# Optimization experiments

Hardware: AMD Instinct MI355X
Metric: run time of the kernel (lower is better)

Reference implementation:

```python
import jax, jax.numpy as jnp
import numpy as np

EPS = 1e-7  # keras.backend.epsilon()
B, U, F = 1024, 256, 31
D = 1 + U + F  # features dim after concat


def setup_inputs() -> dict:
    key = jax.random.key(0)
    ks = jax.random.split(key, 9)
    s = 1.0 / np.sqrt(D)
    return {
        "last_cell": jax.random.uniform(ks[0], (B, U), dtype=jnp.float32),
        "input_precipitation": jax.random.uniform(ks[1], (B,), dtype=jnp.float32),
        "input_other_features": jax.random.normal(ks[2], (B, F), dtype=jnp.float32),
        "W_i": jax.random.normal(ks[3], (D, U), dtype=jnp.float32) * s,
        "b_i": jnp.zeros((U,), dtype=jnp.float32),
        "W_r": jax.random.normal(ks[4], (D, U * U), dtype=jnp.float32) * s,
        "b_r": jnp.zeros((U * U,), dtype=jnp.float32),
        "W_o": jax.random.normal(ks[5], (D, U), dtype=jnp.float32) * s,
        "b_o": jnp.zeros((U,), dtype=jnp.float32),
    }


def reference(last_cell, input_precipitation, input_other_features,
              W_i, b_i, W_r, b_r, W_o, b_o):
    # L1-normalize last cell state (mass fractions)
    l1 = jnp.sum(jnp.abs(last_cell), axis=-1, keepdims=True) + EPS
    last_cell_hat = last_cell / l1
    p = input_precipitation[:, None]  # [B,1]
    features = jnp.concatenate([p, last_cell_hat, input_other_features], axis=-1)  # [B,D]

    # input gate: sigmoid then L1-normalized across units (mass-conserving split)
    ig = jax.nn.sigmoid(features @ W_i + b_i)
    ig = ig / jnp.sum(jnp.abs(ig), axis=-1, keepdims=True)

    # redistribution matrix: relu, reshape [B,U,U], L1-normalize each row
    R = jax.nn.relu(features @ W_r + b_r).reshape(-1, U, U)
    R = R / jnp.sum(jnp.abs(R), axis=-1, keepdims=True)

    # output gate: sigmoid
    og = jax.nn.sigmoid(features @ W_o + b_o)

    cell_in = ig * p                                   # [B,U]
    cell_sys = jnp.einsum('bu,buv->bv', last_cell, R)  # batched (1xU)@(UxU)
    candidate = cell_in + cell_sys
    output = og * candidate
    cell = (1.0 - og) * candidate
    return (cell, output)
```

## Files before the change

kernel.cpp:

```cpp
#include <hip/hip_runtime.h>


#define EPS_L1 1e-7f

constexpr int BB  = 1024;
constexpr int U   = 256;
constexpr int F   = 31;
constexpr int D   = 1 + U + F;
constexpr int NBV = BB * U;
constexpr int NCH = D / 32;
constexpr int UIMGB = NCH * 16384;
constexpr size_t WTB_BYTES  = (size_t)258 * UIMGB;
constexpr size_t FEAT_BYTES = (size_t)BB * D * 2;
constexpr size_t PART_BYTES = (size_t)32 * BB * U * 4;
constexpr size_t NEED_PRIV  = WTB_BYTES + FEAT_BYTES + PART_BYTES;
constexpr int PITCH = 260;

typedef float f32x4 __attribute__((ext_vector_type(4)));
typedef short bf16x8 __attribute__((ext_vector_type(8)));

__device__ __forceinline__ unsigned f2bf(float x) {
  union { float f; unsigned u; } v; v.f = x;
  unsigned r = v.u + 0x7FFFu + ((v.u >> 16) & 1u);
  return r >> 16;
}

#define GLDS16(gp, lp)                                                        \
  __builtin_amdgcn_global_load_lds(                                          \
      (const __attribute__((address_space(1))) void*)(gp),                   \
      (__attribute__((address_space(3))) void*)(lp), 16, 0, 0)

#define MFMA16(a, b, c) __builtin_amdgcn_mfma_f32_16x16x32_bf16((a), (b), (c), 0, 0, 0)

__global__ __launch_bounds__(256) void k_prep(
    const float* __restrict__ lc, const float* __restrict__ p,
    const float* __restrict__ other,
    const float* __restrict__ Wi, const float* __restrict__ Wr,
    const float* __restrict__ Wo,
    short* __restrict__ WtB, short* __restrict__ featImg,
    float* __restrict__ partial) {
  __shared__ short lds[2][32 * PITCH];
  __shared__ float inv_s[64];
  const int bid = blockIdx.x, t = threadIdx.x;

  if (bid < 774) {
    const int u = bid / 3, part = bid % 3;
    const float* src; long ld;
    if (u < 256)       { src = Wr + (size_t)u * 256; ld = 65536; }
    else if (u == 256) { src = Wi; ld = 256; }
    else               { src = Wo; ld = 256; }
    short* dst = WtB + (size_t)u * 73728;
    const int lane = t & 63, wave = t >> 6;
    const int g = lane >> 4, l15 = lane & 15;

#pragma unroll
    for (int cc = 0; cc < 3; ++cc) {
      const int c = part * 3 + cc;
      short* buf = lds[cc & 1];
#pragma unroll
      for (int i = 0; i < 8; ++i) {
        const int f = i * 256 + t;
        const int row = f >> 6, col4 = f & 63;
        const float4 v = *(const float4*)(src + (size_t)(c * 32 + row) * ld + col4 * 4);
        const unsigned lo = f2bf(v.x) | (f2bf(v.y) << 16);
        const unsigned hi = f2bf(v.z) | (f2bf(v.w) << 16);
        unsigned* wp = (unsigned*)&buf[row * PITCH + col4 * 4];
        wp[0] = lo; wp[1] = hi;
      }
      __syncthreads();
#pragma unroll
      for (int i = 0; i < 4; ++i) {
        const int n0 = wave * 4 + i;
        bf16x8 h;
#pragma unroll
        for (int j = 0; j < 8; ++j)
          h[j] = buf[(g * 8 + j) * PITCH + n0 * 16 + l15];
        *(bf16x8*)(dst + (size_t)(c * 16 + n0) * 512 + lane * 8) = h;
      }
      __syncthreads();
    }
  } else if (bid < 790) {
    const int mb = bid - 774;
    const int b0 = mb * 64;
    const int row = t >> 2, q = t & 3;
    const float4* lp = (const float4*)(lc + (size_t)(b0 + row) * 256 + q * 64);
    float s = 0.f;
#pragma unroll
    for (int j = 0; j < 16; ++j) {
      const float4 v = lp[j];
      s += fabsf(v.x) + fabsf(v.y) + fabsf(v.z) + fabsf(v.w);
    }
    s += __shfl_xor(s, 1, 64);
    s += __shfl_xor(s, 2, 64);
    if (q == 0) inv_s[row] = 1.f / (s + EPS_L1);
    __syncthreads();
#pragma unroll
    for (int i = 0; i < 9; ++i) {
      const int idx = i * 256 + t;
      const int reg = idx >> 6, l = idx & 63;
      const int c = reg >> 2, mt = reg & 3;
      const int lrow = mt * 16 + (l & 15);
      const int grow = b0 + lrow;
      const int k0 = c * 32 + (l >> 4) * 8;
      bf16x8 h;
#pragma unroll
      for (int j = 0; j < 8; ++j) {
        const int k = k0 + j;
        float v;
        if (k == 0) v = p[grow];
        else if (k <= 256) v = lc[(size_t)grow * 256 + (k - 1)] * inv_s[lrow];
        else v = other[(size_t)grow * 31 + (k - 257)];
        h[j] = (short)f2bf(v);
      }
      *(bf16x8*)(featImg + (size_t)mb * 18432 + (size_t)reg * 512 + l * 8) = h;
    }
  } else {
    float4* cs4 = (float4*)partial;
    const int base = (bid - 790) * 8192 + t;
    const float4 z = {0.f, 0.f, 0.f, 0.f};
#pragma unroll
    for (int k2 = 0; k2 < 32; ++k2) cs4[base + k2 * 256] = z;
  }
}

template <bool PRIV>
__global__ __launch_bounds__(1024, 4) void k_heavyR7(
    const short* __restrict__ featImg, const short* __restrict__ WtB,
    const float* __restrict__ lc, const float* __restrict__ br,
    float* __restrict__ partial) {
  __shared__ short aT[36864];
  __shared__ float rsum[2][128][12];
  __shared__ float lcs[2][128];

  const int t = threadIdx.x, lane = t & 63, wave = t >> 6;
  const int cq = wave & 7, rh = wave >> 3;
  const int quad = lane >> 4, l15 = lane & 15;
  const int bid = blockIdx.x;
  const int Mb = bid >> 5, ug = bid & 31;
  const int b0 = Mb * 128, u0 = ug * 8;

  {
    const char* gA = (const char*)featImg + (size_t)Mb * 73728;
    char* lA = (char*)aT;
#pragma unroll
    for (int i = 0; i < 5; ++i) {
      const int off = i * 16384 + t * 16;
      if (off < 73728) GLDS16(gA + off, lA + off);
    }
  }

  const char* aB = (const char*)aT + rh * 36864 + lane * 16;
  const char* bB = (const char*)WtB + (size_t)u0 * UIMGB + cq * 2048 + lane * 16;

  f32x4 acc[4][2], outa[4][2];
#pragma unroll
  for (int m = 0; m < 4; ++m)
#pragma unroll
    for (int n = 0; n < 2; ++n)
#pragma unroll
      for (int r = 0; r < 4; ++r) { acc[m][n][r] = 0.f; outa[m][n][r] = 0.f; }

  bf16x8 afr[2][4], bfr[2][2];

#pragma unroll
  for (int n = 0; n < 2; ++n) bfr[0][n] = *(const bf16x8*)(bB + n * 1024);

  __syncthreads();

#pragma unroll
  for (int m = 0; m < 4; ++m) afr[0][m] = *(const bf16x8*)(aB + m * 1024);

  for (int uu = 0; uu < 8; ++uu) {
    const int u = u0 + uu;
    float bv[2];

#pragma unroll
    for (int c = 0; c < 9; ++c) {
      if (c == 0) {
#pragma unroll
        for (int n = 0; n < 2; ++n)
          bv[n] = br[(size_t)u * 256 + cq * 32 + n * 16 + l15];
        if (t < 128) lcs[uu & 1][t] = lc[(size_t)(b0 + t) * 256 + u];
      }
      if (c < 8) {
#pragma unroll
        for (int n = 0; n < 2; ++n)
          bfr[(c + 1) & 1][n] = *(const bf16x8*)(bB + (c + 1) * 16384 + n * 1024);
#pragma unroll
        for (int m = 0; m < 4; ++m)
          afr[(c + 1) & 1][m] = *(const bf16x8*)(aB + (c + 1) * 4096 + m * 1024);
      }
#pragma unroll
      for (int m = 0; m < 4; ++m)
#pragma unroll
        for (int n = 0; n < 2; ++n)
          acc[m][n] = MFMA16(afr[c & 1][m], bfr[c & 1][n], acc[m][n]);
    }
    bB += UIMGB;

#pragma unroll
    for (int n = 0; n < 2; ++n) bfr[0][n] = *(const bf16x8*)(bB + n * 1024);
#pragma unroll
    for (int m = 0; m < 4; ++m) afr[0][m] = *(const bf16x8*)(aB + m * 1024);

    const int ub = uu & 1;
    float sm[4][4];
#pragma unroll
    for (int m = 0; m < 4; ++m)
#pragma unroll
      for (int r = 0; r < 4; ++r) {
        float sv = 0.f;
#pragma unroll
        for (int n = 0; n < 2; ++n) {
          const float rv = fmaxf(acc[m][n][r] + bv[n], 0.f);
          acc[m][n][r] = rv;
          sv += rv;
        }
        sm[m][r] = sv;
      }
#pragma unroll
    for (int msk = 1; msk < 16; msk <<= 1)
#pragma unroll
      for (int m = 0; m < 4; ++m)
#pragma unroll
        for (int r = 0; r < 4; ++r)
          sm[m][r] += __shfl_xor(sm[m][r], msk, 64);
    if (l15 == 0) {
#pragma unroll
      for (int m = 0; m < 4; ++m)
#pragma unroll
        for (int r = 0; r < 4; ++r)
          rsum[ub][rh * 64 + m * 16 + quad * 4 + r][cq] = sm[m][r];
    }
    __syncthreads();
#pragma unroll
    for (int m = 0; m < 4; ++m)
#pragma unroll
      for (int r = 0; r < 4; ++r) {
        const int row = rh * 64 + m * 16 + quad * 4 + r;
        const float4 ra = *(const float4*)&rsum[ub][row][0];
        const float4 rb = *(const float4*)&rsum[ub][row][4];
        const float tot = ((ra.x + ra.y) + (ra.z + ra.w)) +
                          ((rb.x + rb.y) + (rb.z + rb.w));
        const float alpha = lcs[ub][row] * __builtin_amdgcn_rcpf(tot);
#pragma unroll
        for (int n = 0; n < 2; ++n) {
          outa[m][n][r] = fmaf(alpha, acc[m][n][r], outa[m][n][r]);
          acc[m][n][r] = 0.f;
        }
      }
  }

  const size_t pb = PRIV ? ((size_t)ug << 18) : 0;
#pragma unroll
  for (int m = 0; m < 4; ++m)
#pragma unroll
    for (int r = 0; r < 4; ++r) {
      const int grow = b0 + rh * 64 + m * 16 + quad * 4 + r;
      const size_t rb = pb + (size_t)grow * 256 + cq * 32 + l15;
      if (PRIV) {
        partial[rb]      = outa[m][0][r];
        partial[rb + 16] = outa[m][1][r];
      } else {
        atomicAdd(&partial[rb],      outa[m][0][r]);
        atomicAdd(&partial[rb + 16], outa[m][1][r]);
      }
    }
}

__global__ __launch_bounds__(512, 2) void k_postR7(
    const short* __restrict__ featImg, const short* __restrict__ WtB,
    const float* __restrict__ bi, const float* __restrict__ bo,
    const float* __restrict__ p, const float* __restrict__ partial, int npart,
    float* __restrict__ dout) {
  __shared__ short aT9[9 * 512];
  __shared__ float cs[16 * 256];
  __shared__ float rsum[16][12];
  __shared__ float ps[16];

  const int t = threadIdx.x, lane = t & 63, cg = t >> 6;
  const int quad = lane >> 4, l15 = lane & 15;
  const int mb16 = blockIdx.x, b0 = mb16 * 16;
  const int mb = mb16 >> 2, mt = mb16 & 3;

  {
    const char* gsrc = (const char*)featImg + (size_t)mb * 36864 + mt * 1024;
    char* ldst = (char*)aT9;
    GLDS16(gsrc + (size_t)(t >> 6) * 4096 + (t & 63) * 16, ldst + t * 16);
    if (t < 64)
      GLDS16(gsrc + (size_t)8 * 4096 + t * 16, ldst + 8192 + t * 16);
  }
  if (t < 16) ps[t] = p[b0 + t];

  {
    const float* pbase = partial + (size_t)b0 * 256;
    f32x4 s0 = {0.f, 0.f, 0.f, 0.f}, s1 = {0.f, 0.f, 0.f, 0.f};
#pragma unroll 4
    for (int ug = 0; ug < npart; ++ug) {
      const f32x4* pp = (const f32x4*)(pbase + (size_t)ug * 262144);
      s0 += pp[t];
      s1 += pp[512 + t];
    }
    ((f32x4*)cs)[t] = s0;
    ((f32x4*)cs)[512 + t] = s1;
  }

  f32x4 acc[2];
#pragma unroll
  for (int n = 0; n < 2; ++n)
#pragma unroll
    for (int r = 0; r < 4; ++r) acc[n][r] = 0.f;

  const char* bptr = (const char*)WtB + (size_t)256 * UIMGB + cg * 2048 + lane * 16;
  bf16x8 cb0 = *(const bf16x8*)(bptr);
  bf16x8 cb1 = *(const bf16x8*)(bptr + 1024);
  bf16x8 nb0 = *(const bf16x8*)(bptr + 16384);
  bf16x8 nb1 = *(const bf16x8*)(bptr + 16384 + 1024);
  bptr += 32768;

  __syncthreads();

  float ig0[4], ig1[4], og0[4], og1[4];

#pragma unroll
  for (int g = 0; g < 2; ++g) {
    const float* bias = (g == 0) ? bi : bo;
    const float bv0 = bias[cg * 32 + l15];
    const float bv1 = bias[cg * 32 + 16 + l15];
#pragma unroll
    for (int c = 0; c < 9; ++c) {
      const bf16x8 pb0 = *(const bf16x8*)(bptr);
      const bf16x8 pb1 = *(const bf16x8*)(bptr + 1024);
      bptr += 16384;
      const bf16x8 a0 = *(const bf16x8*)((const char*)aT9 + c * 1024 + lane * 16);
      acc[0] = MFMA16(a0, cb0, acc[0]);
      acc[1] = MFMA16(a0, cb1, acc[1]);
      cb0 = nb0; cb1 = nb1; nb0 = pb0; nb1 = pb1;
    }

#pragma unroll
    for (int r = 0; r < 4; ++r) {
      const float v0 = 1.f / (1.f + __expf(-(acc[0][r] + bv0)));
      const float v1 = 1.f / (1.f + __expf(-(acc[1][r] + bv1)));
      if (g == 0) { ig0[r] = v0; ig1[r] = v1; }
      else        { og0[r] = v0; og1[r] = v1; }
      acc[0][r] = 0.f;
      acc[1][r] = 0.f;
    }

    if (g == 0) {
      float sm[4];
#pragma unroll
      for (int r = 0; r < 4; ++r) sm[r] = ig0[r] + ig1[r];
#pragma unroll
      for (int msk = 1; msk < 16; msk <<= 1)
#pragma unroll
        for (int r = 0; r < 4; ++r)
          sm[r] += __shfl_xor(sm[r], msk, 64);
      if (l15 == 0) {
#pragma unroll
        for (int r = 0; r < 4; ++r)
          rsum[quad * 4 + r][cg] = sm[r];
      }
      __syncthreads();
#pragma unroll
      for (int r = 0; r < 4; ++r) {
        const int row = quad * 4 + r;
        const float4 ra = *(const float4*)&rsum[row][0];
        const float4 rb = *(const float4*)&rsum[row][4];
        const float inv = 1.f / (((ra.x + ra.y) + (ra.z + ra.w)) +
                                 ((rb.x + rb.y) + (rb.z + rb.w)));
        ig0[r] *= inv;
        ig1[r] *= inv;
      }
    }
  }

#pragma unroll
  for (int r = 0; r < 4; ++r) {
    const int row = quad * 4 + r;
    const float pr = ps[row];
    const int ci = row * 256 + cg * 32 + l15;
    const size_t base = (size_t)(b0 + row) * 256 + cg * 32 + l15;
    {
      const float cand = fmaf(ig0[r], pr, cs[ci]);
      dout[base] = (1.f - og0[r]) * cand;
      dout[NBV + base] = og0[r] * cand;
    }
    {
      const float cand = fmaf(ig1[r], pr, cs[ci + 16]);
      dout[base + 16] = (1.f - og1[r]) * cand;
      dout[NBV + base + 16] = og1[r] * cand;
    }
  }
}

extern "C" void kernel_launch(void* const* d_in, const int* in_sizes, int n_in,
                              void* d_out, int out_size, void* d_ws, size_t ws_size,
                              hipStream_t stream) {
  const float* lc    = (const float*)d_in[0];
  const float* p     = (const float*)d_in[1];
  const float* other = (const float*)d_in[2];
  const float* Wi    = (const float*)d_in[3];
  const float* bi    = (const float*)d_in[4];
  const float* Wr    = (const float*)d_in[5];
  const float* br    = (const float*)d_in[6];
  const float* Wo    = (const float*)d_in[7];
  const float* bo    = (const float*)d_in[8];
  float* out = (float*)d_out;

  char* wsb = (char*)d_ws;
  short* WtB      = (short*)wsb;
  short* featImg  = (short*)(wsb + WTB_BYTES);
  float* partial  = (float*)(wsb + WTB_BYTES + FEAT_BYTES);
  const bool priv = (ws_size >= NEED_PRIV);

  k_prep<<<798, 256, 0, stream>>>(lc, p, other, Wi, Wr, Wo, WtB, featImg, partial);
  if (priv)
    k_heavyR7<true><<<256, 1024, 0, stream>>>(featImg, WtB, lc, br, partial);
  else
    k_heavyR7<false><<<256, 1024, 0, stream>>>(featImg, WtB, lc, br, partial);
  k_postR7<<<64, 512, 0, stream>>>(featImg, WtB, bi, bo, p, partial,
                                   priv ? 32 : 1, out);
}
```

Before: 249.0 us.

## Restructure weight prep, widen heavy kernel tiles, drop private partials for atomics

The weight-transpose prep now uses one block per (unit, chunk) with a bf16-pair packed LDS transpose, giving about three times as many blocks. The heavy kernel moves from 1024 to 512 threads, so each wave covers 64 output columns (4 N fragments), with triple-buffered B fragments and last_cell values preloaded once. The 32-way private partial buffer is removed. All blocks now atomically add into a single zeroed cell_sys array, which the post kernel reads directly instead of summing 32 partials. This trades a large partial-buffer write and read for more atomics and higher register pressure per wave.

Result: faster. 216.8 us (-12.9%).

```diff
diff --git a/kernel.cpp b/kernel.cpp
--- a/kernel.cpp
+++ b/kernel.cpp
@@ -12,9 +12,6 @@
 constexpr int UIMGB = NCH * 16384;
 constexpr size_t WTB_BYTES  = (size_t)258 * UIMGB;
 constexpr size_t FEAT_BYTES = (size_t)BB * D * 2;
-constexpr size_t PART_BYTES = (size_t)32 * BB * U * 4;
-constexpr size_t NEED_PRIV  = WTB_BYTES + FEAT_BYTES + PART_BYTES;
-constexpr int PITCH = 260;
 
 typedef float f32x4 __attribute__((ext_vector_type(4)));
 typedef short bf16x8 __attribute__((ext_vector_type(8)));
@@ -38,49 +35,47 @@
     const float* __restrict__ Wi, const float* __restrict__ Wr,
     const float* __restrict__ Wo,
     short* __restrict__ WtB, short* __restrict__ featImg,
-    float* __restrict__ partial) {
-  __shared__ short lds[2][32 * PITCH];
+    float* __restrict__ cell_sys) {
+  __shared__ unsigned tw[256][17];
   __shared__ float inv_s[64];
   const int bid = blockIdx.x, t = threadIdx.x;
 
-  if (bid < 774) {
-    const int u = bid / 3, part = bid % 3;
+  if (bid < 2322) {
+    const int u = bid / 9, c = bid % 9;
     const float* src; long ld;
     if (u < 256)       { src = Wr + (size_t)u * 256; ld = 65536; }
     else if (u == 256) { src = Wi; ld = 256; }
     else               { src = Wo; ld = 256; }
-    short* dst = WtB + (size_t)u * 73728;
+
+    const int kp = t >> 4, f = t & 15;
+    const float* r0 = src + (size_t)(c * 32 + 2 * kp) * ld;
+    const float* r1 = r0 + ld;
+#pragma unroll
+    for (int i = 0; i < 4; ++i) {
+      const int v0 = f * 4 + i * 64;
+      const float4 a = *(const float4*)(r0 + v0);
+      const float4 b = *(const float4*)(r1 + v0);
+      tw[v0 + 0][kp] = f2bf(a.x) | (f2bf(b.x) << 16);
+      tw[v0 + 1][kp] = f2bf(a.y) | (f2bf(b.y) << 16);
+      tw[v0 + 2][kp] = f2bf(a.z) | (f2bf(b.z) << 16);
+      tw[v0 + 3][kp] = f2bf(a.w) | (f2bf(b.w) << 16);
+    }
+    __syncthreads();
+
     const int lane = t & 63, wave = t >> 6;
     const int g = lane >> 4, l15 = lane & 15;
-
-#pragma unroll
-    for (int cc = 0; cc < 3; ++cc) {
-      const int c = part * 3 + cc;
-      short* buf = lds[cc & 1];
-#pragma unroll
-      for (int i = 0; i < 8; ++i) {
-        const int f = i * 256 + t;
-        const int row = f >> 6, col4 = f & 63;
-        const float4 v = *(const float4*)(src + (size_t)(c * 32 + row) * ld + col4 * 4);
-        const unsigned lo = f2bf(v.x) | (f2bf(v.y) << 16);
-        const unsigned hi = f2bf(v.z) | (f2bf(v.w) << 16);
-        unsigned* wp = (unsigned*)&buf[row * PITCH + col4 * 4];
-        wp[0] = lo; wp[1] = hi;
-      }
-      __syncthreads();
-#pragma unroll
-      for (int i = 0; i < 4; ++i) {
-        const int n0 = wave * 4 + i;
-        bf16x8 h;
-#pragma unroll
-        for (int j = 0; j < 8; ++j)
-          h[j] = buf[(g * 8 + j) * PITCH + n0 * 16 + l15];
-        *(bf16x8*)(dst + (size_t)(c * 16 + n0) * 512 + lane * 8) = h;
-      }
-      __syncthreads();
-    }
-  } else if (bid < 790) {
-    const int mb = bid - 774;
+    short* dst = WtB + (size_t)u * 73728 + (size_t)c * 16 * 512;
+#pragma unroll
+    for (int ii = 0; ii < 4; ++ii) {
+      const int n0 = wave * 4 + ii;
+      const int row = n0 * 16 + l15;
+      union { unsigned u4[4]; bf16x8 h; } cv;
+#pragma unroll
+      for (int j = 0; j < 4; ++j) cv.u4[j] = tw[row][g * 4 + j];
+      *(bf16x8*)(dst + (size_t)n0 * 512 + lane * 8) = cv.h;
+    }
+  } else if (bid < 2338) {
+    const int mb = bid - 2322;
     const int b0 = mb * 64;
     const int row = t >> 2, q = t & 3;
     const float4* lp = (const float4*)(lc + (size_t)(b0 + row) * 256 + q * 64);
@@ -115,25 +110,24 @@
       *(bf16x8*)(featImg + (size_t)mb * 18432 + (size_t)reg * 512 + l * 8) = h;
     }
   } else {
-    float4* cs4 = (float4*)partial;
-    const int base = (bid - 790) * 8192 + t;
+    float4* cs4 = (float4*)cell_sys;
+    const int base = (bid - 2338) * 8192 + t;
     const float4 z = {0.f, 0.f, 0.f, 0.f};
 #pragma unroll
     for (int k2 = 0; k2 < 32; ++k2) cs4[base + k2 * 256] = z;
   }
 }
 
-template <bool PRIV>
-__global__ __launch_bounds__(1024, 4) void k_heavyR7(
+__global__ __launch_bounds__(512, 2) void k_heavyR8(
     const short* __restrict__ featImg, const short* __restrict__ WtB,
     const float* __restrict__ lc, const float* __restrict__ br,
-    float* __restrict__ partial) {
+    float* __restrict__ cell_sys) {
   __shared__ short aT[36864];
-  __shared__ float rsum[2][128][12];
-  __shared__ float lcs[2][128];
+  __shared__ float rsum[2][128][4];
+  __shared__ float lcs[8][128];
 
   const int t = threadIdx.x, lane = t & 63, wave = t >> 6;
-  const int cq = wave & 7, rh = wave >> 3;
+  const int cq = wave & 3, rh = wave >> 2;
   const int quad = lane >> 4, l15 = lane & 15;
   const int bid = blockIdx.x;
   const int Mb = bid >> 5, ug = bid & 31;
@@ -143,49 +137,56 @@
     const char* gA = (const char*)featImg + (size_t)Mb * 73728;
     char* lA = (char*)aT;
 #pragma unroll
-    for (int i = 0; i < 5; ++i) {
-      const int off = i * 16384 + t * 16;
-      if (off < 73728) GLDS16(gA + off, lA + off);
-    }
+    for (int i = 0; i < 9; ++i)
+      GLDS16(gA + i * 8192 + t * 16, lA + i * 8192 + t * 16);
+  }
+
+  if (t < 128) {
+    const float* lp = lc + (size_t)(b0 + t) * 256 + u0;
+    const float4 v0 = *(const float4*)(lp);
+    const float4 v1 = *(const float4*)(lp + 4);
+    lcs[0][t] = v0.x; lcs[1][t] = v0.y; lcs[2][t] = v0.z; lcs[3][t] = v0.w;
+    lcs[4][t] = v1.x; lcs[5][t] = v1.y; lcs[6][t] = v1.z; lcs[7][t] = v1.w;
   }
 
   const char* aB = (const char*)aT + rh * 36864 + lane * 16;
-  const char* bB = (const char*)WtB + (size_t)u0 * UIMGB + cq * 2048 + lane * 16;
-
-  f32x4 acc[4][2], outa[4][2];
+  const char* bB = (const char*)WtB + (size_t)u0 * UIMGB + cq * 4096 + lane * 16;
+
+  f32x4 acc[4][4], outa[4][4];
 #pragma unroll
   for (int m = 0; m < 4; ++m)
 #pragma unroll
-    for (int n = 0; n < 2; ++n)
+    for (int n = 0; n < 4; ++n)
 #pragma unroll
       for (int r = 0; r < 4; ++r) { acc[m][n][r] = 0.f; outa[m][n][r] = 0.f; }
 
-  bf16x8 afr[2][4], bfr[2][2];
-
-#pragma unroll
-  for (int n = 0; n < 2; ++n) bfr[0][n] = *(const bf16x8*)(bB + n * 1024);
+  bf16x8 bfr[3][4];
+#pragma unroll
+  for (int n = 0; n < 4; ++n) bfr[0][n] = *(const bf16x8*)(bB + n * 1024);
+#pragma unroll
+  for (int n = 0; n < 4; ++n) bfr[1][n] = *(const bf16x8*)(bB + 16384 + n * 1024);
 
   __syncthreads();
 
+  bf16x8 afr[2][4];
 #pragma unroll
   for (int m = 0; m < 4; ++m) afr[0][m] = *(const bf16x8*)(aB + m * 1024);
 
   for (int uu = 0; uu < 8; ++uu) {
     const int u = u0 + uu;
-    float bv[2];
+    float bv[4];
 
 #pragma unroll
     for (int c = 0; c < 9; ++c) {
       if (c == 0) {
 #pragma unroll
-        for (int n = 0; n < 2; ++n)
-          bv[n] = br[(size_t)u * 256 + cq * 32 + n * 16 + l15];
-        if (t < 128) lcs[uu & 1][t] = lc[(size_t)(b0 + t) * 256 + u];
-      }
+        for (int n = 0; n < 4; ++n)
+          bv[n] = br[(size_t)u * 256 + cq * 64 + n * 16 + l15];
+      }
+#pragma unroll
+      for (int n = 0; n < 4; ++n)
+        bfr[(c + 2) % 3][n] = *(const bf16x8*)(bB + (c + 2) * 16384 + n * 1024);
       if (c < 8) {
-#pragma unroll
-        for (int n = 0; n < 2; ++n)
-          bfr[(c + 1) & 1][n] = *(const bf16x8*)(bB + (c + 1) * 16384 + n * 1024);
 #pragma unroll
         for (int m = 0; m < 4; ++m)
           afr[(c + 1) & 1][m] = *(const bf16x8*)(aB + (c + 1) * 4096 + m * 1024);
@@ -193,13 +194,11 @@
 #pragma unroll
       for (int m = 0; m < 4; ++m)
 #pragma unroll
-        for (int n = 0; n < 2; ++n)
-          acc[m][n] = MFMA16(afr[c & 1][m], bfr[c & 1][n], acc[m][n]);
+        for (int n = 0; n < 4; ++n)
+          acc[m][n] = MFMA16(afr[c & 1][m], bfr[c % 3][n], acc[m][n]);
     }
     bB += UIMGB;
 
-#pragma unroll
-    for (int n = 0; n < 2; ++n) bfr[0][n] = *(const bf16x8*)(bB + n * 1024);
 #pragma unroll
     for (int m = 0; m < 4; ++m) afr[0][m] = *(const bf16x8*)(aB + m * 1024);
 
@@ -211,7 +210,7 @@
       for (int r = 0; r < 4; ++r) {
         float sv = 0.f;
 #pragma unroll
-        for (int n = 0; n < 2; ++n) {
+        for (int n = 0; n < 4; ++n) {
           const float rv = fmaxf(acc[m][n][r] + bv[n], 0.f);
           acc[m][n][r] = rv;
           sv += rv;
@@ -238,40 +237,33 @@
 #pragma unroll
       for (int r = 0; r < 4; ++r) {
         const int row = rh * 64 + m * 16 + quad * 4 + r;
-        const float4 ra = *(const float4*)&rsum[ub][row][0];
-        const float4 rb = *(const float4*)&rsum[ub][row][4];
-        const float tot = ((ra.x + ra.y) + (ra.z + ra.w)) +
-                          ((rb.x + rb.y) + (rb.z + rb.w));
-        const float alpha = lcs[ub][row] * __builtin_amdgcn_rcpf(tot);
-#pragma unroll
-        for (int n = 0; n < 2; ++n) {
+        const float4 rv = *(const float4*)&rsum[ub][row][0];
+        const float tot = (rv.x + rv.y) + (rv.z + rv.w);
+        const float alpha = lcs[uu][row] * __builtin_amdgcn_rcpf(tot);
+#pragma unroll
+        for (int n = 0; n < 4; ++n) {
           outa[m][n][r] = fmaf(alpha, acc[m][n][r], outa[m][n][r]);
           acc[m][n][r] = 0.f;
         }
       }
   }
 
-  const size_t pb = PRIV ? ((size_t)ug << 18) : 0;
 #pragma unroll
   for (int m = 0; m < 4; ++m)
 #pragma unroll
     for (int r = 0; r < 4; ++r) {
       const int grow = b0 + rh * 64 + m * 16 + quad * 4 + r;
-      const size_t rb = pb + (size_t)grow * 256 + cq * 32 + l15;
-      if (PRIV) {
-        partial[rb]      = outa[m][0][r];
-        partial[rb + 16] = outa[m][1][r];
-      } else {
-        atomicAdd(&partial[rb],      outa[m][0][r]);
-        atomicAdd(&partial[rb + 16], outa[m][1][r]);
-      }
+#pragma unroll
+      for (int n = 0; n < 4; ++n)
+        atomicAdd(&cell_sys[(size_t)grow * 256 + cq * 64 + n * 16 + l15],
+                  outa[m][n][r]);
     }
 }
 
-__global__ __launch_bounds__(512, 2) void k_postR7(
+__global__ __launch_bounds__(512, 2) void k_postR8(
     const short* __restrict__ featImg, const short* __restrict__ WtB,
     const float* __restrict__ bi, const float* __restrict__ bo,
-    const float* __restrict__ p, const float* __restrict__ partial, int npart,
+    const float* __restrict__ p, const float* __restrict__ cell_sys,
     float* __restrict__ dout) {
   __shared__ short aT9[9 * 512];
   __shared__ float cs[16 * 256];
@@ -293,16 +285,9 @@
   if (t < 16) ps[t] = p[b0 + t];
 
   {
-    const float* pbase = partial + (size_t)b0 * 256;
-    f32x4 s0 = {0.f, 0.f, 0.f, 0.f}, s1 = {0.f, 0.f, 0.f, 0.f};
-#pragma unroll 4
-    for (int ug = 0; ug < npart; ++ug) {
-      const f32x4* pp = (const f32x4*)(pbase + (size_t)ug * 262144);
-      s0 += pp[t];
-      s1 += pp[512 + t];
-    }
-    ((f32x4*)cs)[t] = s0;
-    ((f32x4*)cs)[512 + t] = s1;
+    const f32x4* pp = (const f32x4*)(cell_sys + (size_t)b0 * 256);
+    ((f32x4*)cs)[t] = pp[t];
+    ((f32x4*)cs)[512 + t] = pp[512 + t];
   }
 
   f32x4 acc[2];
@@ -412,14 +397,9 @@
   char* wsb = (char*)d_ws;
   short* WtB      = (short*)wsb;
   short* featImg  = (short*)(wsb + WTB_BYTES);
-  float* partial  = (float*)(wsb + WTB_BYTES + FEAT_BYTES);
-  const bool priv = (ws_size >= NEED_PRIV);
-
-  k_prep<<<798, 256, 0, stream>>>(lc, p, other, Wi, Wr, Wo, WtB, featImg, partial);
-  if (priv)
-    k_heavyR7<true><<<256, 1024, 0, stream>>>(featImg, WtB, lc, br, partial);
-  else
-    k_heavyR7<false><<<256, 1024, 0, stream>>>(featImg, WtB, lc, br, partial);
-  k_postR7<<<64, 512, 0, stream>>>(featImg, WtB, bi, bo, p, partial,
-                                   priv ? 32 : 1, out);
+  float* cell_sys = (float*)(wsb + WTB_BYTES + FEAT_BYTES);
+
+  k_prep<<<2346, 256, 0, stream>>>(lc, p, other, Wi, Wr, Wo, WtB, featImg, cell_sys);
+  k_heavyR8<<<256, 512, 0, stream>>>(featImg, WtB, lc, br, cell_sys);
+  k_postR8<<<64, 512, 0, stream>>>(featImg, WtB, bi, bo, p, cell_sys, out);
 }
```
